# Optimization experiments

Measured on AMD Instinct MI355X. Metric: run time of the kernel, lower is better.

Reference implementation:

```python
import jax, jax.numpy as jnp
import numpy as np

B, C_IN, C_OUT, H, K = 64, 64, 128, 1855, 6


def setup_inputs() -> dict:
    key = jax.random.key(0)
    k1, k2, k3, k4 = jax.random.split(key, 4)
    x = jax.random.normal(k1, (B, C_IN, H), dtype=jnp.float32)
    # neighbor table [H, K]; valid indices first, -1 padding at the end
    neighbors = jax.random.randint(k2, (H, K), 0, H)
    n_boundary = H // 10
    neighbors = neighbors.at[:n_boundary, K - 2:].set(-1)
    weight_center = jax.random.normal(k3, (C_OUT, C_IN), dtype=jnp.float32) / np.sqrt(C_IN).astype(np.float32)
    weight_neighbors = jax.random.normal(k4, (C_OUT, C_IN, K), dtype=jnp.float32) / np.sqrt(C_IN * K).astype(np.float32)
    bias = jnp.zeros((C_OUT,), dtype=jnp.float32)
    return {
        "x": x,
        "neighbors": neighbors,
        "weight_center": weight_center,
        "weight_neighbors": weight_neighbors,
        "bias": bias,
    }


def reference(x, neighbors, weight_center, weight_neighbors, bias):
    # x: [B, C_in, H]; neighbors: [H, K] with -1 = invalid (valid-first ordering)
    mask = neighbors >= 0                               # [H, K]
    idx = jnp.where(mask, neighbors, 0)                 # safe gather indices
    gathered = x[:, :, idx] * mask.astype(x.dtype)[None, None, :, :]  # [B, C_in, H, K]
    center = jnp.einsum('bch,oc->boh', x, weight_center)              # [B, C_out, H]
    neigh = jnp.einsum('bchk,ock->boh', gathered, weight_neighbors)   # [B, C_out, H]
    counts = (1 + mask.sum(axis=-1)).astype(x.dtype)                  # [H]
    return (center + neigh) / counts[None, None, :] + bias[None, :, None]
```

## Files before the change

kernel.cpp:

```cpp
#include <hip/hip_runtime.h>
#include <hip/hip_bf16.h>
#include <stdint.h>

typedef __bf16 bf16x8 __attribute__((ext_vector_type(8)));
typedef float floatx4 __attribute__((ext_vector_type(4)));
typedef unsigned short u16;
typedef unsigned int u32;

#define B_    64
#define CIN   64
#define COUT  128
#define H_    1855
#define KNB   6
#define KTOT  448
#define NSTEPS 14
#define TILE_H 64
#define RS    456
#define NTILES 29

#define XT_OFF   0
#define XT_BYTES ((size_t)H_ * 4096 * 2)
#define WP_OFF   XT_BYTES
#define WP_BYTES ((size_t)COUT * KTOT * 2)
#define FLAG_OFF (WP_OFF + WP_BYTES)

static __device__ inline u16 f32_to_bf16(float f) {
    u32 u = __float_as_uint(f);
    u32 r = (u + 0x7FFFu + ((u >> 16) & 1u)) >> 16;
    return (u16)r;
}
static __device__ inline float bf16_to_f32(u16 b) {
    return __uint_as_float(((u32)b) << 16);
}

__global__ __launch_bounds__(256) void k_detect(const u32* __restrict__ x,
                                                int* __restrict__ flag) {
    __shared__ int votes;
    if (threadIdx.x == 0) votes = 0;
    __syncthreads();
    int cnt = 0;
#pragma unroll
    for (int i = 0; i < 4; ++i) {
        u32 w = x[threadIdx.x * 4 + i];
        u32 e = (w >> 7) & 0xFFu;
        cnt += (e >= 115u && e <= 131u) ? 1 : 0;
    }
    atomicAdd(&votes, cnt);
    __syncthreads();
    if (threadIdx.x == 0) *flag = (votes >= 512) ? 1 : 0;
}

__global__ __launch_bounds__(256) void k_transpose(const void* __restrict__ x,
                                                   u16* __restrict__ xt,
                                                   const int* __restrict__ flag) {
    int isBf = *flag;
    __shared__ u16 tile[64][65];
    int h0  = blockIdx.x * 64;
    int bc0 = blockIdx.y * 64;
    int lane = threadIdx.x & 63;
    int rowq = threadIdx.x >> 6;
#pragma unroll
    for (int i = 0; i < 16; ++i) {
        int row = i * 4 + rowq;
        int h = h0 + lane;
        u16 v = 0;
        if (h < H_) {
            size_t idx = (size_t)(bc0 + row) * H_ + h;
            v = isBf ? ((const u16*)x)[idx] : f32_to_bf16(((const float*)x)[idx]);
        }
        tile[row][lane] = v;
    }
    __syncthreads();
#pragma unroll
    for (int i = 0; i < 16; ++i) {
        int hr = i * 4 + rowq;
        int h = h0 + hr;
        if (h < H_) xt[(size_t)h * 4096 + bc0 + lane] = tile[lane][hr];
    }
}

__global__ __launch_bounds__(256) void k_pack(const void* __restrict__ wc,
                                              const void* __restrict__ wn,
                                              u16* __restrict__ wp,
                                              const int* __restrict__ flag) {
    int isBf = *flag;
    int tg = blockIdx.x * 256 + threadIdx.x;
    if (tg >= COUT * KTOT) return;
    int o = tg / KTOT;
    int rem = tg - o * KTOT;
    int s = rem >> 6, c = rem & 63;
    int srcIdx = (s == 0) ? (o * CIN + c) : ((o * CIN + c) * KNB + (s - 1));
    u16 v;
    if (s == 0) v = isBf ? ((const u16*)wc)[srcIdx] : f32_to_bf16(((const float*)wc)[srcIdx]);
    else        v = isBf ? ((const u16*)wn)[srcIdx] : f32_to_bf16(((const float*)wn)[srcIdx]);
    wp[tg] = v;
}

__global__ __launch_bounds__(256, 2) void k_main(const u16* __restrict__ xt,
                                                 const u16* __restrict__ wp,
                                                 const int* __restrict__ nbr,
                                                 const void* __restrict__ bias,
                                                 const int* __restrict__ flag,
                                                 void* __restrict__ out) {
    __shared__ __align__(16) u16 X[TILE_H * RS];
    __shared__ float cInv[TILE_H];

    int isBf = *flag;
    int tid  = threadIdx.x;
    int b    = blockIdx.x >> 3;
    int slot = blockIdx.x & 7;
    int lane = tid & 63;
    int wave = tid >> 6;
    int col  = lane & 15;
    int quad = lane >> 4;
    int m0w  = wave * 32;

    bf16x8 afrag[2][NSTEPS];
#pragma unroll
    for (int mt = 0; mt < 2; ++mt) {
        int o = m0w + mt * 16 + col;
#pragma unroll
        for (int kk = 0; kk < NSTEPS; ++kk) {
            afrag[mt][kk] = *(const bf16x8*)(wp + o * KTOT + kk * 32 + quad * 8);
        }
    }
    float biasv[2][4];
#pragma unroll
    for (int mt = 0; mt < 2; ++mt)
#pragma unroll
        for (int r = 0; r < 4; ++r) {
            int o = m0w + mt * 16 + quad * 4 + r;
            biasv[mt][r] = isBf ? bf16_to_f32(((const u16*)bias)[o])
                                : ((const float*)bias)[o];
        }

    for (int t = slot; t < NTILES; t += 8) {
        int h0 = t * TILE_H;
        __syncthreads();

        if (tid < TILE_H) {
            int h = h0 + tid;
            int cnt = 1;
            if (h < H_) {
#pragma unroll
                for (int j = 0; j < KNB; ++j) cnt += (nbr[h * KNB + j] >= 0) ? 1 : 0;
            }
            cInv[tid] = 1.0f / (float)cnt;
        }

#pragma unroll
        for (int s = 0; s < 7; ++s) {
#pragma unroll
            for (int r = 0; r < 2; ++r) {
                int idx = r * 256 + tid;
                int hl = idx >> 3;
                int chunk = idx & 7;
                int h = h0 + hl;
                int src = -1;
                if (h < H_) src = (s == 0) ? h : nbr[h * KNB + (s - 1)];
                uint4 v = make_uint4(0u, 0u, 0u, 0u);
                if (src >= 0 && src < H_)
                    v = *(const uint4*)(xt + (size_t)src * 4096 + b * 64 + chunk * 8);
                *(uint4*)(X + hl * RS + s * 64 + chunk * 8) = v;
            }
        }
        __syncthreads();

        floatx4 acc[2][4];
#pragma unroll
        for (int mt = 0; mt < 2; ++mt)
#pragma unroll
            for (int nt = 0; nt < 4; ++nt)
                acc[mt][nt] = (floatx4){0.0f, 0.0f, 0.0f, 0.0f};

#pragma unroll
        for (int kk = 0; kk < NSTEPS; ++kk) {
            bf16x8 bfr[4];
#pragma unroll
            for (int nt = 0; nt < 4; ++nt)
                bfr[nt] = *(const bf16x8*)(X + (nt * 16 + col) * RS + kk * 32 + quad * 8);
#pragma unroll
            for (int mt = 0; mt < 2; ++mt)
#pragma unroll
                for (int nt = 0; nt < 4; ++nt)
                    acc[mt][nt] = __builtin_amdgcn_mfma_f32_16x16x32_bf16(
                        afrag[mt][kk], bfr[nt], acc[mt][nt], 0, 0, 0);
        }

#pragma unroll
        for (int nt = 0; nt < 4; ++nt) {
            int h = h0 + nt * 16 + col;
            if (h < H_) {
                float ic = cInv[nt * 16 + col];
#pragma unroll
                for (int mt = 0; mt < 2; ++mt)
#pragma unroll
                    for (int r = 0; r < 4; ++r) {
                        int o = m0w + mt * 16 + quad * 4 + r;
                        float v = acc[mt][nt][r] * ic + biasv[mt][r];
                        size_t oi = ((size_t)b * COUT + o) * H_ + h;
                        if (isBf) ((u16*)out)[oi] = f32_to_bf16(v);
                        else      ((float*)out)[oi] = v;
                    }
            }
        }
    }
}

extern "C" void kernel_launch(void* const* d_in, const int* in_sizes, int n_in,
                              void* d_out, int out_size, void* d_ws, size_t ws_size,
                              hipStream_t stream) {
    const void* x    = d_in[0];
    const int*  nbr  = (const int*)d_in[1];
    const void* wc   = d_in[2];
    const void* wn   = d_in[3];
    const void* bias = d_in[4];

    u16* xt  = (u16*)((char*)d_ws + XT_OFF);
    u16* wp  = (u16*)((char*)d_ws + WP_OFF);
    int* flg = (int*)((char*)d_ws + FLAG_OFF);

    k_detect<<<dim3(1), dim3(256), 0, stream>>>((const u32*)x, flg);
    k_pack<<<dim3((COUT * KTOT) / 256), dim3(256), 0, stream>>>(wc, wn, wp, flg);
    k_transpose<<<dim3(NTILES, 64), dim3(256), 0, stream>>>(x, xt, flg);
    k_main<<<dim3(512), dim3(256), 0, stream>>>(xt, wp, nbr, bias, flg, (u16*)d_out);
}
```

Before: 155.6 us.

## Per-batch transposed layout, inline dtype detection, staged coalesced output, XCD-aware grid

Drops the separate detection kernel and instead has each kernel sample 16 input words to decide the dtype. Reorganizes the transposed x buffer as [B][H][64] so each batch's gathered rows are contiguous, and remaps blocks so a batch's tiles share one XCD's L2. The grid grows to 960 blocks handling two tiles each, and results are staged through shared memory for coalesced row-wise global stores. The new detection heuristic uses fewer samples, which risks misclassifying the dtype, and the staging adds extra barriers.

```diff
diff --git a/kernel.cpp b/kernel.cpp
--- a/kernel.cpp
+++ b/kernel.cpp
@@ -18,12 +18,6 @@
 #define RS    456
 #define NTILES 29
 
-#define XT_OFF   0
-#define XT_BYTES ((size_t)H_ * 4096 * 2)
-#define WP_OFF   XT_BYTES
-#define WP_BYTES ((size_t)COUT * KTOT * 2)
-#define FLAG_OFF (WP_OFF + WP_BYTES)
-
 static __device__ inline u16 f32_to_bf16(float f) {
     u32 u = __float_as_uint(f);
     u32 r = (u + 0x7FFFu + ((u >> 16) & 1u)) >> 16;
@@ -32,97 +26,98 @@
 static __device__ inline float bf16_to_f32(u16 b) {
     return __uint_as_float(((u32)b) << 16);
 }
-
-__global__ __launch_bounds__(256) void k_detect(const u32* __restrict__ x,
-                                                int* __restrict__ flag) {
-    __shared__ int votes;
-    if (threadIdx.x == 0) votes = 0;
-    __syncthreads();
+static __device__ inline int detect16(const u32* __restrict__ x) {
     int cnt = 0;
 #pragma unroll
-    for (int i = 0; i < 4; ++i) {
-        u32 w = x[threadIdx.x * 4 + i];
-        u32 e = (w >> 7) & 0xFFu;
+    for (int i = 0; i < 16; ++i) {
+        u32 e = (x[i] >> 7) & 0xFFu;
         cnt += (e >= 115u && e <= 131u) ? 1 : 0;
     }
-    atomicAdd(&votes, cnt);
-    __syncthreads();
-    if (threadIdx.x == 0) *flag = (votes >= 512) ? 1 : 0;
+    return cnt >= 12;
 }
 
 __global__ __launch_bounds__(256) void k_transpose(const void* __restrict__ x,
-                                                   u16* __restrict__ xt,
-                                                   const int* __restrict__ flag) {
-    int isBf = *flag;
+                                                   u16* __restrict__ xt2) {
+    int isBf = detect16((const u32*)x);
     __shared__ u16 tile[64][65];
-    int h0  = blockIdx.x * 64;
-    int bc0 = blockIdx.y * 64;
+    int h0 = blockIdx.x * 64;
+    int b  = blockIdx.y;
     int lane = threadIdx.x & 63;
     int rowq = threadIdx.x >> 6;
+    const u16*   xb16 = (const u16*)x + (size_t)b * CIN * H_;
+    const float* xb32 = (const float*)x + (size_t)b * CIN * H_;
+    int h = h0 + lane;
+    bool hv = h < H_;
 #pragma unroll
     for (int i = 0; i < 16; ++i) {
-        int row = i * 4 + rowq;
-        int h = h0 + lane;
+        int c = i * 4 + rowq;
         u16 v = 0;
-        if (h < H_) {
-            size_t idx = (size_t)(bc0 + row) * H_ + h;
-            v = isBf ? ((const u16*)x)[idx] : f32_to_bf16(((const float*)x)[idx]);
-        }
-        tile[row][lane] = v;
+        if (hv) v = isBf ? xb16[c * H_ + h] : f32_to_bf16(xb32[c * H_ + h]);
+        tile[c][lane] = v;
     }
     __syncthreads();
 #pragma unroll
     for (int i = 0; i < 16; ++i) {
         int hr = i * 4 + rowq;
-        int h = h0 + hr;
-        if (h < H_) xt[(size_t)h * 4096 + bc0 + lane] = tile[lane][hr];
+        int hh = h0 + hr;
+        if (hh < H_)
+            xt2[((size_t)b * H_ + hh) * 64 + lane] = tile[lane][hr];
     }
 }
 
 __global__ __launch_bounds__(256) void k_pack(const void* __restrict__ wc,
                                               const void* __restrict__ wn,
                                               u16* __restrict__ wp,
-                                              const int* __restrict__ flag) {
-    int isBf = *flag;
+                                              const u32* __restrict__ xraw) {
+    int isBf = detect16(xraw);
     int tg = blockIdx.x * 256 + threadIdx.x;
     if (tg >= COUT * KTOT) return;
     int o = tg / KTOT;
     int rem = tg - o * KTOT;
     int s = rem >> 6, c = rem & 63;
-    int srcIdx = (s == 0) ? (o * CIN + c) : ((o * CIN + c) * KNB + (s - 1));
     u16 v;
-    if (s == 0) v = isBf ? ((const u16*)wc)[srcIdx] : f32_to_bf16(((const float*)wc)[srcIdx]);
-    else        v = isBf ? ((const u16*)wn)[srcIdx] : f32_to_bf16(((const float*)wn)[srcIdx]);
+    if (s == 0) {
+        int si = o * CIN + c;
+        v = isBf ? ((const u16*)wc)[si] : f32_to_bf16(((const float*)wc)[si]);
+    } else {
+        int si = (o * CIN + c) * KNB + (s - 1);
+        v = isBf ? ((const u16*)wn)[si] : f32_to_bf16(((const float*)wn)[si]);
+    }
     wp[tg] = v;
 }
 
-__global__ __launch_bounds__(256, 2) void k_main(const u16* __restrict__ xt,
+__global__ __launch_bounds__(256, 2) void k_main(const u16* __restrict__ xt2,
                                                  const u16* __restrict__ wp,
                                                  const int* __restrict__ nbr,
                                                  const void* __restrict__ bias,
-                                                 const int* __restrict__ flag,
-                                                 void* __restrict__ out) {
+                                                 void* __restrict__ out,
+                                                 const u32* __restrict__ xraw) {
     __shared__ __align__(16) u16 X[TILE_H * RS];
     __shared__ float cInv[TILE_H];
 
-    int isBf = *flag;
+    int isBf = detect16(xraw);
     int tid  = threadIdx.x;
-    int b    = blockIdx.x >> 3;
-    int slot = blockIdx.x & 7;
+    int g    = blockIdx.x;
+    int xcd  = g & 7;
+    int j    = g >> 3;
+    int b    = xcd * 8 + (j & 7);
+    int T    = j >> 3;
+
     int lane = tid & 63;
     int wave = tid >> 6;
     int col  = lane & 15;
     int quad = lane >> 4;
     int m0w  = wave * 32;
 
+    const u16* xb = xt2 + (size_t)b * (H_ * 64);
+
     bf16x8 afrag[2][NSTEPS];
 #pragma unroll
     for (int mt = 0; mt < 2; ++mt) {
         int o = m0w + mt * 16 + col;
 #pragma unroll
-        for (int kk = 0; kk < NSTEPS; ++kk) {
+        for (int kk = 0; kk < NSTEPS; ++kk)
             afrag[mt][kk] = *(const bf16x8*)(wp + o * KTOT + kk * 32 + quad * 8);
-        }
     }
     float biasv[2][4];
 #pragma unroll
@@ -134,7 +129,10 @@
                                 : ((const float*)bias)[o];
         }
 
-    for (int t = slot; t < NTILES; t += 8) {
+#pragma unroll
+    for (int tt = 0; tt < 2; ++tt) {
+        int t = T * 2 + tt;
+        if (t >= NTILES) break;
         int h0 = t * TILE_H;
         __syncthreads();
 
@@ -143,24 +141,27 @@
             int cnt = 1;
             if (h < H_) {
 #pragma unroll
-                for (int j = 0; j < KNB; ++j) cnt += (nbr[h * KNB + j] >= 0) ? 1 : 0;
+                for (int jj = 0; jj < KNB; ++jj) cnt += (nbr[h * KNB + jj] >= 0) ? 1 : 0;
             }
             cInv[tid] = 1.0f / (float)cnt;
         }
 
 #pragma unroll
-        for (int s = 0; s < 7; ++s) {
-#pragma unroll
-            for (int r = 0; r < 2; ++r) {
-                int idx = r * 256 + tid;
-                int hl = idx >> 3;
-                int chunk = idx & 7;
-                int h = h0 + hl;
-                int src = -1;
-                if (h < H_) src = (s == 0) ? h : nbr[h * KNB + (s - 1)];
+        for (int r = 0; r < 2; ++r) {
+            int idx = r * 256 + tid;
+            int hl = idx >> 3, chunk = idx & 7;
+            int h = h0 + hl;
+            bool hv = h < H_;
+            int srcs[7];
+            srcs[0] = hv ? h : -1;
+#pragma unroll
+            for (int s = 1; s < 7; ++s)
+                srcs[s] = hv ? nbr[h * KNB + s - 1] : -1;
+#pragma unroll
+            for (int s = 0; s < 7; ++s) {
                 uint4 v = make_uint4(0u, 0u, 0u, 0u);
-                if (src >= 0 && src < H_)
-                    v = *(const uint4*)(xt + (size_t)src * 4096 + b * 64 + chunk * 8);
+                if (srcs[s] >= 0)
+                    v = *(const uint4*)(xb + (size_t)srcs[s] * 64 + chunk * 8);
                 *(uint4*)(X + hl * RS + s * 64 + chunk * 8) = v;
             }
         }
@@ -187,21 +188,48 @@
                         afrag[mt][kk], bfr[nt], acc[mt][nt], 0, 0, 0);
         }
 
-#pragma unroll
-        for (int nt = 0; nt < 4; ++nt) {
-            int h = h0 + nt * 16 + col;
-            if (h < H_) {
+        __syncthreads();
+        int hmax = (H_ - h0 < TILE_H) ? (H_ - h0) : TILE_H;
+        if (isBf) {
+            u16* stage = X;
+#pragma unroll
+            for (int nt = 0; nt < 4; ++nt) {
                 float ic = cInv[nt * 16 + col];
 #pragma unroll
                 for (int mt = 0; mt < 2; ++mt)
 #pragma unroll
                     for (int r = 0; r < 4; ++r) {
                         int o = m0w + mt * 16 + quad * 4 + r;
-                        float v = acc[mt][nt][r] * ic + biasv[mt][r];
-                        size_t oi = ((size_t)b * COUT + o) * H_ + h;
-                        if (isBf) ((u16*)out)[oi] = f32_to_bf16(v);
-                        else      ((float*)out)[oi] = v;
+                        stage[o * 72 + nt * 16 + col] =
+                            f32_to_bf16(acc[mt][nt][r] * ic + biasv[mt][r]);
                     }
+            }
+            __syncthreads();
+            u16* ob = (u16*)out + (size_t)b * COUT * H_ + h0;
+#pragma unroll
+            for (int rr = 0; rr < 32; ++rr) {
+                int o = m0w + rr;
+                if (lane < hmax) ob[(size_t)o * H_ + lane] = stage[o * 72 + lane];
+            }
+        } else {
+            float* stage = (float*)X;
+#pragma unroll
+            for (int nt = 0; nt < 4; ++nt) {
+                float ic = cInv[nt * 16 + col];
+#pragma unroll
+                for (int mt = 0; mt < 2; ++mt)
+#pragma unroll
+                    for (int r = 0; r < 4; ++r) {
+                        int o = m0w + mt * 16 + quad * 4 + r;
+                        stage[o * 68 + nt * 16 + col] = acc[mt][nt][r] * ic + biasv[mt][r];
+                    }
+            }
+            __syncthreads();
+            float* ob = (float*)out + (size_t)b * COUT * H_ + h0;
+#pragma unroll
+            for (int rr = 0; rr < 32; ++rr) {
+                int o = m0w + rr;
+                if (lane < hmax) ob[(size_t)o * H_ + lane] = stage[o * 68 + lane];
             }
         }
     }
@@ -216,12 +244,10 @@
     const void* wn   = d_in[3];
     const void* bias = d_in[4];
 
-    u16* xt  = (u16*)((char*)d_ws + XT_OFF);
-    u16* wp  = (u16*)((char*)d_ws + WP_OFF);
-    int* flg = (int*)((char*)d_ws + FLAG_OFF);
-
-    k_detect<<<dim3(1), dim3(256), 0, stream>>>((const u32*)x, flg);
-    k_pack<<<dim3((COUT * KTOT) / 256), dim3(256), 0, stream>>>(wc, wn, wp, flg);
-    k_transpose<<<dim3(NTILES, 64), dim3(256), 0, stream>>>(x, xt, flg);
-    k_main<<<dim3(512), dim3(256), 0, stream>>>(xt, wp, nbr, bias, flg, (u16*)d_out);
-}
+    u16* xt2 = (u16*)d_ws;
+    u16* wp  = (u16*)((char*)d_ws + (size_t)B_ * H_ * 64 * 2);
+
+    k_pack<<<dim3((COUT * KTOT) / 256), dim3(256), 0, stream>>>(wc, wn, wp, (const u32*)x);
+    k_transpose<<<dim3(NTILES, B_), dim3(256), 0, stream>>>(x, xt2);
+    k_main<<<dim3(960), dim3(256), 0, stream>>>(xt2, wp, nbr, bias, d_out, (const u32*)x);
+}
```

After: 146.8 us. -5.7%, faster.
